# Kernel tuning notes

Measured on AMD Instinct MI355X. Metric: run time of the kernel, lower is better.

## Reference

```python
import jax, jax.numpy as jnp
import numpy as np

B, N, D, K = 1024, 36, 256, 8  # batch, num_features(fixed 36 by docstring), embed_size, text_K


def setup_inputs() -> dict:
    key = jax.random.key(0)
    ks = jax.random.split(key, 5)
    texts = jax.random.normal(ks[0], (B, N, D), dtype=jnp.float32)
    # Xavier-uniform-style init matching module.init_weights()
    r_k = np.sqrt(6.0) / np.sqrt(D + D)
    r_v = np.sqrt(6.0) / np.sqrt(D + K)
    r_u = np.sqrt(6.0) / np.sqrt(K + 1)
    W = jax.random.uniform(ks[1], (K, D, D), minval=-r_k, maxval=r_k, dtype=jnp.float32)
    Wb = jnp.zeros((K, D), dtype=jnp.float32)
    V1w = jax.random.uniform(ks[2], (K, D), minval=-r_v, maxval=r_v, dtype=jnp.float32)
    V1b = jnp.zeros((K,), dtype=jnp.float32)
    V2w = jax.random.uniform(ks[3], (K, D), minval=-r_v, maxval=r_v, dtype=jnp.float32)
    V2b = jnp.zeros((K,), dtype=jnp.float32)
    Uw = jax.random.uniform(ks[4], (K,), minval=-r_u, maxval=r_u, dtype=jnp.float32)
    Ub = jnp.zeros((), dtype=jnp.float32)
    return {"texts": texts, "W": W, "Wb": Wb, "V1w": V1w, "V1b": V1b,
            "V2w": V2w, "V2b": V2b, "Uw": Uw, "Ub": Ub}


def reference(texts, W, Wb, V1w, V1b, V2w, V2b, Uw, Ub):
    # bilinear term: (W_k x_n + b_k) . x_m  -> [B,K,N,N]
    Wx = jnp.einsum('kcd,bnd->bknc', W, texts) + Wb[None, :, None, :]
    first = jnp.einsum('bknc,bmc->bknm', Wx, texts)
    # outer-sum term: V1.x_n + V2.x_m (per k)
    v1 = jnp.einsum('kd,bnd->bkn', V1w, texts) + V1b[None, :, None]  # [B,K,N]
    v2 = jnp.einsum('kd,bmd->bkm', V2w, texts) + V2b[None, :, None]  # [B,K,N]
    T = jnp.tanh(first + v1[..., None] + v2[:, :, None, :])  # [B,K,N,N]
    # faithful to torch: flatten [K,N,N] contiguously then view as (N*N, K)
    flat = T.reshape(T.shape[0], N * N, K)
    logits = (flat @ Uw + Ub).reshape(T.shape[0], N, N)
    return jax.nn.softmax(logits, axis=-1)
```

## Files before the change

kernel.cpp:

```cpp
#include <hip/hip_runtime.h>
#include <math.h>

#define NB 1024
#define NF 36
#define ED 256
#define NK 8
#define NN2 1296
#define QPK 162

typedef _Float16 f16;
typedef f16 f16x4 __attribute__((ext_vector_type(4)));
typedef f16 f16x8 __attribute__((ext_vector_type(8)));
typedef float f32x4 __attribute__((ext_vector_type(4)));

#define WXSTR 136
#define WXHSZ 13056
#define NFRAG 1536

#define XH_OFF  0
#define WXH_OFF 24576
#define V_OFF   (24576 + WXHSZ)
#define SMEM_MAIN (V_OFF + (72 + 72 + 9 + 324) * 4)

#define PVH_OFF 0
#define PVL_OFF 8192
#define PP_OFF  16384
#define SMEM_PREP 28672

#define TWO_LOG2E 2.8853900817779268f
#define C1F (0.0625f * TWO_LOG2E)

__device__ __forceinline__ f32x4 mfma16(f16x8 a, f16x8 b, f32x4 c) {
    return __builtin_amdgcn_mfma_f32_16x16x32_f16(a, b, c, 0, 0, 0);
}

__global__ __launch_bounds__(256, 4) void prep_all(
    const float* __restrict__ W, f16x8* __restrict__ WfH,
    const float* __restrict__ texts, f16x8* __restrict__ XfH,
    const float* __restrict__ V1w, const float* __restrict__ V1b,
    const float* __restrict__ V2w, const float* __restrict__ V2b,
    const float* __restrict__ Wb, float* __restrict__ v12)
{
    extern __shared__ char psmem[];
    const int blk = blockIdx.x;
    const int t = threadIdx.x;
    const int wave = t >> 6, lane = t & 63;

    if (blk < 128) {
        const int k = blk >> 4, ct = blk & 15;
        f16* Wl = (f16*)psmem;
        {
            const int r = t >> 4, seg = t & 15;
            const float* src = W + ((size_t)(k * 256 + ct * 16 + r)) * 256 + seg * 16;
            f16* d = Wl + r * 264 + seg * 16;
            #pragma unroll
            for (int j4 = 0; j4 < 4; ++j4) {
                float4 a = ((const float4*)src)[j4];
                d[j4 * 4 + 0] = (f16)(a.x * 16.0f);
                d[j4 * 4 + 1] = (f16)(a.y * 16.0f);
                d[j4 * 4 + 2] = (f16)(a.z * 16.0f);
                d[j4 * 4 + 3] = (f16)(a.w * 16.0f);
            }
        }
        __syncthreads();
        f16x8* dst = WfH + (size_t)(k * 16 + ct) * 8 * 64;
        #pragma unroll
        for (int e0 = 0; e0 < 2; ++e0) {
            const int e = t + e0 * 256;
            const int kc = e >> 6, el = e & 63, qd = el >> 4, l15 = el & 15;
            dst[e] = *(const f16x8*)(Wl + l15 * 264 + (kc * 4 + qd) * 8);
        }
        return;
    }

    f16x8* VfH = (f16x8*)(psmem + PVH_OFF);
    f16x8* VfL = (f16x8*)(psmem + PVL_OFF);
    f32x4* Pp  = (f32x4*)(psmem + PP_OFF);

    const int b = blk - 128;
    const float* xb = texts + (size_t)b * NF * ED;

    #pragma unroll
    for (int i0 = 0; i0 < 2; ++i0) {
        int i = t + i0 * 256;
        int kc = (i >> 6) & 7, ln = i & 63;
        int q = ln >> 4, col = ln & 15;
        int which = col >> 3, kk = col & 7;
        const float* src  = (which ? V2w : V1w) + kk * 256 + kc * 32 + q * 8;
        const float* srcb = Wb + kk * 256 + kc * 32 + q * 8;
        f16x8 hi, lo;
        #pragma unroll
        for (int j = 0; j < 8; ++j) {
            float sv = src[j] + (which ? srcb[j] : 0.f);
            sv *= 16.0f;
            f16 h = (f16)sv;
            hi[j] = h;
            lo[j] = (f16)(sv - (float)h);
        }
        VfH[i] = hi;
        VfL[i] = lo;
    }

    f16x8 FH[6], FL[6];
    #pragma unroll
    for (int i0 = 0; i0 < 6; ++i0) {
        int i = t + i0 * 256;
        int rt = i >> 9, kc = (i >> 6) & 7;
        int q = lane >> 4, l15 = lane & 15;
        int row = rt * 16 + l15;
        f16x8 hi, lo;
        if (row < NF) {
            const float* s = xb + row * ED + kc * 32 + q * 8;
            float4 a = *(const float4*)s;
            float4 c = *(const float4*)(s + 4);
            float v[8] = {a.x, a.y, a.z, a.w, c.x, c.y, c.z, c.w};
            #pragma unroll
            for (int j = 0; j < 8; ++j) {
                f16 h = (f16)v[j];
                hi[j] = h;
                lo[j] = (f16)(v[j] - (float)h);
            }
        } else {
            #pragma unroll
            for (int j = 0; j < 8; ++j) { hi[j] = (f16)0.f; lo[j] = (f16)0.f; }
        }
        FH[i0] = hi;
        FL[i0] = lo;
        XfH[(size_t)b * NFRAG + i] = hi;
    }
    __syncthreads();

    f32x4 pacc[3];
    #pragma unroll
    for (int rt = 0; rt < 3; ++rt) pacc[rt] = (f32x4){0.f, 0.f, 0.f, 0.f};
    #pragma unroll
    for (int rt = 0; rt < 3; ++rt) {
        #pragma unroll
        for (int s = 0; s < 2; ++s) {
            const int i0 = rt * 2 + s;
            const int kc = wave + 4 * s;
            f16x8 bh = VfH[kc * 64 + lane];
            f16x8 bl = VfL[kc * 64 + lane];
            pacc[rt] = mfma16(FH[i0], bh, pacc[rt]);
            pacc[rt] = mfma16(FH[i0], bl, pacc[rt]);
            pacc[rt] = mfma16(FL[i0], bh, pacc[rt]);
        }
    }
    #pragma unroll
    for (int rt = 0; rt < 3; ++rt)
        Pp[(wave * 3 + rt) * 64 + lane] = pacc[rt];
    __syncthreads();

    if (wave < 3) {
        f32x4 acc = Pp[(0 * 3 + wave) * 64 + lane];
        #pragma unroll
        for (int w = 1; w < 4; ++w) acc += Pp[(w * 3 + wave) * 64 + lane];
        const int q = lane >> 4, l15 = lane & 15;
        const int which = l15 >> 3, kk = l15 & 7;
        const float bias = which ? V2b[kk] : V1b[kk];
        #pragma unroll
        for (int r = 0; r < 4; ++r) {
            const int n = wave * 16 + q * 4 + r;
            if (n < NF)
                v12[((size_t)b * 16 + l15) * NF + n] = acc[r] * 0.0625f + bias;
        }
    }
}

__global__ __launch_bounds__(256, 4) void ntn_main(
    const f16x8* __restrict__ XfHG,
    const f16x8* __restrict__ WfH,
    const float* __restrict__ v12,
    const float* __restrict__ Uw, const float* __restrict__ Ubp,
    float* __restrict__ out)
{
    extern __shared__ char smem[];
    f16x8* Xh   = (f16x8*)(smem + XH_OFF);
    f16*   Wxh  = (f16*)(smem + WXH_OFF);
    float* v1s2 = (float*)(smem + V_OFF);
    float* v2s2 = v1s2 + 72;
    float* Uws  = v1s2 + 144;
    float* Ls   = v1s2 + 153;

    const int id  = blockIdx.x;
    const int xcd = id & 7;
    const int rem = id >> 3;
    const int kp  = rem & 3;
    const int b   = ((rem >> 2) << 3) | xcd;
    const int k0  = kp * 2;

    const int t    = threadIdx.x;
    const int wave = t >> 6;
    const int lane = t & 63;
    const int quad = lane >> 4;
    const int l15  = lane & 15;

    {
        const f16x8* gh = XfHG + (size_t)b * NFRAG;
        #pragma unroll
        for (int i = 0; i < 6; ++i) Xh[t + i * 256] = gh[t + i * 256];
    }
    if (t < 144) {
        const int r = t / 36, n = t - r * 36;
        const int which = r & 1, kq = r >> 1;
        float v = v12[((size_t)b * 16 + which * 8 + (k0 + kq)) * NF + n] * TWO_LOG2E;
        (which ? v2s2 : v1s2)[kq * 36 + n] = v;
    }
    if (t < 8) Uws[t] = Uw[t];
    if (t == 8) Uws[8] = Ubp[0];
    __syncthreads();

    const f16x8* Wk0 = WfH + (size_t)k0 * 8192;
    const f16x8* Wk1 = Wk0 + 8192;

    f32x4 sacc[2][3];
    #pragma unroll
    for (int kk = 0; kk < 2; ++kk)
        #pragma unroll
        for (int it = 0; it < 3; ++it) sacc[kk][it] = (f32x4){0.f, 0.f, 0.f, 0.f};

    for (int h = 0; h < 2; ++h) {
        f32x4 acc[3][2][2];
        #pragma unroll
        for (int i = 0; i < 3; ++i)
            #pragma unroll
            for (int j = 0; j < 2; ++j) {
                acc[i][j][0] = (f32x4){0.f, 0.f, 0.f, 0.f};
                acc[i][j][1] = (f32x4){0.f, 0.f, 0.f, 0.f};
            }
        const int ct0 = h * 8 + wave;
        const int ct1 = ct0 + 4;
        #pragma unroll 2
        for (int kc = 0; kc < 8; ++kc) {
            f16x8 w00 = Wk0[(ct0 * 8 + kc) * 64 + lane];
            f16x8 w01 = Wk0[(ct1 * 8 + kc) * 64 + lane];
            f16x8 w10 = Wk1[(ct0 * 8 + kc) * 64 + lane];
            f16x8 w11 = Wk1[(ct1 * 8 + kc) * 64 + lane];
            #pragma unroll
            for (int rt = 0; rt < 3; ++rt) {
                f16x8 ah = Xh[(rt * 8 + kc) * 64 + lane];
                acc[rt][0][0] = mfma16(w00, ah, acc[rt][0][0]);
                acc[rt][1][0] = mfma16(w01, ah, acc[rt][1][0]);
                acc[rt][0][1] = mfma16(w10, ah, acc[rt][0][1]);
                acc[rt][1][1] = mfma16(w11, ah, acc[rt][1][1]);
            }
        }
        #pragma unroll
        for (int kk = 0; kk < 2; ++kk) {
            __syncthreads();
            #pragma unroll
            for (int rt = 0; rt < 3; ++rt) {
                const int n = rt * 16 + l15;
                #pragma unroll
                for (int j2 = 0; j2 < 2; ++j2) {
                    const int cb = (j2 ? (wave + 4) : wave) * 16 + quad * 4;
                    f16x4 h4;
                    #pragma unroll
                    for (int r = 0; r < 4; ++r) h4[r] = (f16)(acc[rt][j2][kk][r]);
                    *(f16x4*)(Wxh + n * WXSTR + cb) = h4;
                }
            }
            __syncthreads();
            #pragma unroll
            for (int it = 0; it < 3; ++it) {
                const int p = wave + it * 4;
                if (p < 9) {
                    const int nt = p / 3, mt = p % 3;
                    const f16* wxh_p = Wxh + (nt * 16 + l15) * WXSTR + quad * 8;
                    #pragma unroll
                    for (int kc2 = 0; kc2 < 4; ++kc2) {
                        f16x8 pah = *(const f16x8*)(wxh_p + kc2 * 32);
                        f16x8 pbh = Xh[(mt * 8 + h * 4 + kc2) * 64 + lane];
                        sacc[kk][it] = mfma16(pah, pbh, sacc[kk][it]);
                    }
                }
            }
        }
    }

    __syncthreads();
    float* Ts = (float*)Wxh;
    #pragma unroll
    for (int kk = 0; kk < 2; ++kk)
        #pragma unroll
        for (int it = 0; it < 3; ++it) {
            const int p = wave + it * 4;
            if (p < 9) {
                const int nt = p / 3, mt = p % 3;
                const int m = mt * 16 + l15;
                if (m < NF) {
                    #pragma unroll
                    for (int r = 0; r < 4; ++r) {
                        const int n = nt * 16 + quad * 4 + r;
                        if (n < NF) {
                            float x = sacc[kk][it][r] * C1F
                                      + v1s2[kk * 36 + n] + v2s2[kk * 36 + m];
                            float e = exp2f(x);
                            const int idx = kk * NN2 + n * NF + m;
                            Ts[idx + (idx >> 3)] = 1.f - 2.f / (e + 1.f);
                        }
                    }
                }
            }
        }
    __syncthreads();
    #pragma unroll
    for (int u0 = 0; u0 < 2; ++u0) {
        const int u = t + u0 * 256;
        if (u < 324) {
            const float* tp = Ts + u * 9;
            float lg = Uws[8];
            #pragma unroll
            for (int j = 0; j < 8; ++j) lg += Uws[j] * tp[j];
            Ls[u] = lg;
        }
    }
    __syncthreads();
    #pragma unroll
    for (int rr0 = 0; rr0 < 3; ++rr0) {
        const int rr = wave + rr0 * 4;
        if (rr < 9) {
            float v = (lane < NF) ? Ls[rr * 36 + lane] : -INFINITY;
            float mx = v;
            #pragma unroll
            for (int off = 32; off > 0; off >>= 1) mx = fmaxf(mx, __shfl_xor(mx, off));
            float e = (lane < NF) ? __expf(v - mx) : 0.f;
            float sm = e;
            #pragma unroll
            for (int off = 32; off > 0; off >>= 1) sm += __shfl_xor(sm, off);
            if (lane < NF)
                out[(size_t)b * NN2 + kp * 324 + rr * 36 + lane] = e / sm;
        }
    }
}

extern "C" void kernel_launch(void* const* d_in, const int* in_sizes, int n_in,
                              void* d_out, int out_size, void* d_ws, size_t ws_size,
                              hipStream_t stream) {
    const float* texts = (const float*)d_in[0];
    const float* W     = (const float*)d_in[1];
    const float* Wb    = (const float*)d_in[2];
    const float* V1w   = (const float*)d_in[3];
    const float* V1b   = (const float*)d_in[4];
    const float* V2w   = (const float*)d_in[5];
    const float* V2b   = (const float*)d_in[6];
    const float* Uw    = (const float*)d_in[7];
    const float* Ub    = (const float*)d_in[8];

    char* ws = (char*)d_ws;
    f16x8* WfH = (f16x8*)ws;
    f16x8* XfH = (f16x8*)(ws + (1 << 20));
    float* v12 = (float*)(ws + (1 << 20) + (size_t)NB * NFRAG * 16);
    float* outp = (float*)d_out;

    hipFuncSetAttribute((const void*)prep_all,
                        hipFuncAttributeMaxDynamicSharedMemorySize, SMEM_PREP);
    hipFuncSetAttribute((const void*)ntn_main,
                        hipFuncAttributeMaxDynamicSharedMemorySize, SMEM_MAIN);

    prep_all<<<128 + NB, 256, SMEM_PREP, stream>>>(W, WfH, texts, XfH,
                                                   V1w, V1b, V2w, V2b, Wb, v12);
    ntn_main<<<NB * NK / 2, 256, SMEM_MAIN, stream>>>(XfH, WfH, v12, Uw, Ub, outp);
}
```

Baseline: 186.5 us.

## Software-pipeline Wx GEMM segments with interleaved bilinear MFMA tiles

Reorganizes the main loop into four segments, one per (k, half) pair. Each segment computes one k's half of Wx while interleaving the previous segment's second-stage MFMA tiles, which read the staged Wxh in shared memory. The goal is to hide LDS-dependent phase-2 work and barrier stalls behind phase-1 global loads and MFMAs. It also halves the live accumulator registers, which may help occupancy. The cost is more barriers and fully unrolled code.

```diff
diff --git a/kernel.cpp b/kernel.cpp
--- a/kernel.cpp
+++ b/kernel.cpp
@@ -166,6 +166,64 @@
         }
     }
 }
+
+#define P1_STEP(ACC, WKP, H, KC) do {                                         \
+    f16x8 w0_ = (WKP)[((((H) * 8 + wave) * 8) + (KC)) * 64 + lane];           \
+    f16x8 w1_ = (WKP)[((((H) * 8 + wave + 4) * 8) + (KC)) * 64 + lane];       \
+    _Pragma("unroll")                                                         \
+    for (int rt_ = 0; rt_ < 3; ++rt_) {                                       \
+        f16x8 ah_ = Xh[(rt_ * 8 + (KC)) * 64 + lane];                         \
+        ACC[rt_][0] = mfma16(w0_, ah_, ACC[rt_][0]);                          \
+        ACC[rt_][1] = mfma16(w1_, ah_, ACC[rt_][1]);                          \
+    }                                                                         \
+} while (0)
+
+#define P2_TILE(IT, H, KK) do {                                               \
+    const int p_ = wave + (IT) * 4;                                           \
+    if (p_ < 9) {                                                             \
+        const int nt_ = p_ / 3, mt_ = p_ % 3;                                 \
+        const f16* wp_ = Wxh + (nt_ * 16 + l15) * WXSTR + quad * 8;           \
+        _Pragma("unroll")                                                     \
+        for (int kc2_ = 0; kc2_ < 4; ++kc2_) {                                \
+            f16x8 pah_ = *(const f16x8*)(wp_ + kc2_ * 32);                    \
+            f16x8 pbh_ = Xh[(mt_ * 8 + (H) * 4 + kc2_) * 64 + lane];          \
+            sacc[KK][IT] = mfma16(pah_, pbh_, sacc[KK][IT]);                  \
+        }                                                                     \
+    }                                                                         \
+} while (0)
+
+#define ZERO_ACC(ACC) do {                                                    \
+    _Pragma("unroll")                                                         \
+    for (int i_ = 0; i_ < 3; ++i_) {                                          \
+        ACC[i_][0] = (f32x4){0.f, 0.f, 0.f, 0.f};                             \
+        ACC[i_][1] = (f32x4){0.f, 0.f, 0.f, 0.f};                             \
+    }                                                                         \
+} while (0)
+
+#define STORE_WX(ACC) do {                                                    \
+    _Pragma("unroll")                                                         \
+    for (int rt_ = 0; rt_ < 3; ++rt_) {                                       \
+        const int n_ = rt_ * 16 + l15;                                        \
+        _Pragma("unroll")                                                     \
+        for (int j2_ = 0; j2_ < 2; ++j2_) {                                   \
+            const int cb_ = (j2_ ? (wave + 4) : wave) * 16 + quad * 4;        \
+            f16x4 h4_;                                                        \
+            _Pragma("unroll")                                                 \
+            for (int r_ = 0; r_ < 4; ++r_) h4_[r_] = (f16)(ACC[rt_][j2_][r_]);\
+            *(f16x4*)(Wxh + n_ * WXSTR + cb_) = h4_;                          \
+        }                                                                     \
+    }                                                                         \
+} while (0)
+
+#define SEG_FUSED(ACC, WKP, H1, HP, KKP) do {                                 \
+    _Pragma("unroll")                                                         \
+    for (int kc_ = 0; kc_ < 8; ++kc_) {                                       \
+        P1_STEP(ACC, WKP, H1, kc_);                                           \
+        if (kc_ == 1) P2_TILE(0, HP, KKP);                                    \
+        if (kc_ == 3) P2_TILE(1, HP, KKP);                                    \
+        if (kc_ == 5) P2_TILE(2, HP, KKP);                                    \
+    }                                                                         \
+} while (0)
 
 __global__ __launch_bounds__(256, 4) void ntn_main(
     const f16x8* __restrict__ XfHG,
@@ -219,64 +277,35 @@
         #pragma unroll
         for (int it = 0; it < 3; ++it) sacc[kk][it] = (f32x4){0.f, 0.f, 0.f, 0.f};
 
-    for (int h = 0; h < 2; ++h) {
-        f32x4 acc[3][2][2];
-        #pragma unroll
-        for (int i = 0; i < 3; ++i)
-            #pragma unroll
-            for (int j = 0; j < 2; ++j) {
-                acc[i][j][0] = (f32x4){0.f, 0.f, 0.f, 0.f};
-                acc[i][j][1] = (f32x4){0.f, 0.f, 0.f, 0.f};
-            }
-        const int ct0 = h * 8 + wave;
-        const int ct1 = ct0 + 4;
-        #pragma unroll 2
-        for (int kc = 0; kc < 8; ++kc) {
-            f16x8 w00 = Wk0[(ct0 * 8 + kc) * 64 + lane];
-            f16x8 w01 = Wk0[(ct1 * 8 + kc) * 64 + lane];
-            f16x8 w10 = Wk1[(ct0 * 8 + kc) * 64 + lane];
-            f16x8 w11 = Wk1[(ct1 * 8 + kc) * 64 + lane];
-            #pragma unroll
-            for (int rt = 0; rt < 3; ++rt) {
-                f16x8 ah = Xh[(rt * 8 + kc) * 64 + lane];
-                acc[rt][0][0] = mfma16(w00, ah, acc[rt][0][0]);
-                acc[rt][1][0] = mfma16(w01, ah, acc[rt][1][0]);
-                acc[rt][0][1] = mfma16(w10, ah, acc[rt][0][1]);
-                acc[rt][1][1] = mfma16(w11, ah, acc[rt][1][1]);
-            }
-        }
-        #pragma unroll
-        for (int kk = 0; kk < 2; ++kk) {
-            __syncthreads();
-            #pragma unroll
-            for (int rt = 0; rt < 3; ++rt) {
-                const int n = rt * 16 + l15;
-                #pragma unroll
-                for (int j2 = 0; j2 < 2; ++j2) {
-                    const int cb = (j2 ? (wave + 4) : wave) * 16 + quad * 4;
-                    f16x4 h4;
-                    #pragma unroll
-                    for (int r = 0; r < 4; ++r) h4[r] = (f16)(acc[rt][j2][kk][r]);
-                    *(f16x4*)(Wxh + n * WXSTR + cb) = h4;
-                }
-            }
-            __syncthreads();
-            #pragma unroll
-            for (int it = 0; it < 3; ++it) {
-                const int p = wave + it * 4;
-                if (p < 9) {
-                    const int nt = p / 3, mt = p % 3;
-                    const f16* wxh_p = Wxh + (nt * 16 + l15) * WXSTR + quad * 8;
-                    #pragma unroll
-                    for (int kc2 = 0; kc2 < 4; ++kc2) {
-                        f16x8 pah = *(const f16x8*)(wxh_p + kc2 * 32);
-                        f16x8 pbh = Xh[(mt * 8 + h * 4 + kc2) * 64 + lane];
-                        sacc[kk][it] = mfma16(pah, pbh, sacc[kk][it]);
-                    }
-                }
-            }
-        }
-    }
+    f32x4 acc[3][2];
+
+    ZERO_ACC(acc);
+    #pragma unroll
+    for (int kc = 0; kc < 8; ++kc) P1_STEP(acc, Wk0, 0, kc);
+    STORE_WX(acc);
+    __syncthreads();
+
+    ZERO_ACC(acc);
+    SEG_FUSED(acc, Wk1, 0, 0, 0);
+    __syncthreads();
+    STORE_WX(acc);
+    __syncthreads();
+
+    ZERO_ACC(acc);
+    SEG_FUSED(acc, Wk0, 1, 0, 1);
+    __syncthreads();
+    STORE_WX(acc);
+    __syncthreads();
+
+    ZERO_ACC(acc);
+    SEG_FUSED(acc, Wk1, 1, 1, 0);
+    __syncthreads();
+    STORE_WX(acc);
+    __syncthreads();
+
+    P2_TILE(0, 1, 1);
+    P2_TILE(1, 1, 1);
+    P2_TILE(2, 1, 1);
 
     __syncthreads();
     float* Ts = (float*)Wxh;
```

After: 182.0 us. -2.4%, faster.
